# Performance work log

Hardware: AMD Instinct MI355X
Metric: run time of the kernel (lower is better)

Reference implementation:

```python
import jax, jax.numpy as jnp
import numpy as np


def setup_inputs() -> dict:
    key = jax.random.key(0)
    k1, k2, k3, k4 = jax.random.split(key, 4)
    T, H, E, I = 4096, 1024, 8, 3584
    return {
        "hidden_states": jax.random.normal(k1, (T, H), dtype=jnp.float32),
        "gate_w": jax.random.normal(k2, (H, E), dtype=jnp.float32) * 0.02,
        "w1": jax.random.normal(k3, (E, H, I), dtype=jnp.float32) * 0.02,
        "w2": jax.random.normal(k4, (E, I, H), dtype=jnp.float32) * 0.02,
        "top_k": 2,
    }


def reference(hidden_states, gate_w, w1, w2, top_k):
    # Router: logits -> softmax -> top-k -> renormalize (Mixtral / vLLM fused_moe)
    router_logits = hidden_states @ gate_w                    # [T, E]
    probs = jax.nn.softmax(router_logits, axis=-1)
    top_vals, top_idx = jax.lax.top_k(probs, top_k)           # [T, K]
    top_vals = top_vals / jnp.sum(top_vals, axis=-1, keepdims=True)
    E = gate_w.shape[1]
    # Dense per-(token, expert) combine weights, zero for non-selected experts
    dense_w = jnp.sum(jax.nn.one_hot(top_idx, E, dtype=hidden_states.dtype)
                      * top_vals[..., None], axis=1)          # [T, E]
    # Expert MLP: silu(x @ w1[e]) @ w2[e], weighted by routing probs
    act = jax.nn.silu(jnp.einsum('th,ehi->tei', hidden_states, w1))  # [T, E, I]
    act = act * dense_w[:, :, None]
    out = jnp.einsum('tei,eih->th', act, w2)                  # [T, H]
    return out
```

## Files before the change

kernel.cpp:

```cpp
#include <hip/hip_runtime.h>
#include <hip/hip_bf16.h>

#define T_TOK 4096
#define H_DIM 1024
#define E_NUM 8
#define I_DIM 3584
#define NPAIR (T_TOK * 2)
#define MAX_RT 72

#define BM 128
#define BN 128
#define BK 64

typedef __attribute__((ext_vector_type(8))) short bf16x8;
typedef __attribute__((ext_vector_type(4))) float f32x4;
typedef __attribute__((ext_vector_type(8))) unsigned short ushort8_t;
typedef __attribute__((ext_vector_type(4))) unsigned short ushort4_t;

__device__ __forceinline__ unsigned short f2bf(float x) {
  unsigned int u = __float_as_uint(x);
  unsigned int r = (u + 0x7FFFu + ((u >> 16) & 1u)) >> 16;
  return (unsigned short)r;
}

__device__ __forceinline__ void gload16(const void* g, unsigned short* l) {
  __builtin_amdgcn_global_load_lds(
      (const __attribute__((address_space(1))) void*)g,
      (__attribute__((address_space(3))) void*)l, 16, 0, 0);
}

__device__ __forceinline__ void transpose_body2(const float* __restrict__ src,
                                                unsigned short* __restrict__ dst,
                                                int R, int C, int e, int c0, int r0,
                                                char* smem) {
  float (*tile)[65] = reinterpret_cast<float (*)[65]>(smem);
  const float* s = src + (size_t)e * R * C;
  unsigned short* d = dst + (size_t)e * R * C;
  const int th = threadIdx.x;
  const int tr = th >> 4;
  const int tc4 = (th & 15) * 4;
  const int wc = th >> 3;
  const int wr = (th & 7) * 8;
  ushort8_t oA[2];
#pragma unroll
  for (int it = 0; it < 4; ++it) {
    const int r = it * 16 + tr;
    float4 v = *reinterpret_cast<const float4*>(s + (size_t)(r0 + r) * C + c0 + tc4);
    tile[r][tc4] = v.x; tile[r][tc4 + 1] = v.y; tile[r][tc4 + 2] = v.z; tile[r][tc4 + 3] = v.w;
  }
  __syncthreads();
#pragma unroll
  for (int it = 0; it < 2; ++it) {
    const int c = it * 32 + wc;
#pragma unroll
    for (int j = 0; j < 8; ++j) oA[it][j] = f2bf(tile[wr + j][c]);
  }
  __syncthreads();
#pragma unroll
  for (int it = 0; it < 4; ++it) {
    const int r = it * 16 + tr;
    float4 v = *reinterpret_cast<const float4*>(s + (size_t)(r0 + 64 + r) * C + c0 + tc4);
    tile[r][tc4] = v.x; tile[r][tc4 + 1] = v.y; tile[r][tc4 + 2] = v.z; tile[r][tc4 + 3] = v.w;
  }
  __syncthreads();
#pragma unroll
  for (int it = 0; it < 2; ++it) {
    const int c = it * 32 + wc;
    ushort8_t oB;
#pragma unroll
    for (int j = 0; j < 8; ++j) oB[j] = f2bf(tile[wr + j][c]);
    *reinterpret_cast<ushort8_t*>(d + (size_t)(c0 + c) * R + r0 + wr) = oA[it];
    *reinterpret_cast<ushort8_t*>(d + (size_t)(c0 + c) * R + r0 + 64 + wr) = oB;
  }
}

__device__ __forceinline__ void router_body(const float* __restrict__ hs,
                                            const float* __restrict__ gw,
                                            unsigned short* __restrict__ hsb,
                                            int* __restrict__ eid, float* __restrict__ wgt,
                                            int* __restrict__ counts, int rbid, char* smem) {
  float* s_gw = reinterpret_cast<float*>(smem);
  int* s_cnt = reinterpret_cast<int*>(smem + 32768);
  const int th = threadIdx.x;
  for (int u = th; u < 2048; u += 256) {
    const f32x4 v = *reinterpret_cast<const f32x4*>(gw + u * 4);
    *reinterpret_cast<f32x4*>(&s_gw[(u ^ ((u >> 3) & 7)) * 4]) = v;
  }
  if (th < E_NUM) s_cnt[th] = 0;
  __syncthreads();

  const int l = th & 63, w = th >> 6;
#pragma unroll 1
  for (int tt = 0; tt < 4; ++tt) {
    const int t = rbid * 16 + w * 4 + tt;
    const float* hrow = hs + (size_t)t * H_DIM;
    unsigned short* brow = hsb + (size_t)t * H_DIM;
    float acc[E_NUM];
#pragma unroll
    for (int e = 0; e < E_NUM; ++e) acc[e] = 0.f;
#pragma unroll
    for (int i = 0; i < 4; ++i) {
      const int h0 = i * 256 + l * 4;
      const f32x4 x = *reinterpret_cast<const f32x4*>(hrow + h0);
      ushort4_t o = { f2bf(x[0]), f2bf(x[1]), f2bf(x[2]), f2bf(x[3]) };
      *reinterpret_cast<ushort4_t*>(brow + h0) = o;
#pragma unroll
      for (int j = 0; j < 4; ++j) {
        const int h = h0 + j;
        const int p0 = (h * 2) ^ ((h >> 2) & 7);
        const f32x4 g0 = *reinterpret_cast<const f32x4*>(&s_gw[p0 * 4]);
        const f32x4 g1 = *reinterpret_cast<const f32x4*>(&s_gw[(p0 ^ 1) * 4]);
        acc[0] += x[j] * g0[0]; acc[1] += x[j] * g0[1];
        acc[2] += x[j] * g0[2]; acc[3] += x[j] * g0[3];
        acc[4] += x[j] * g1[0]; acc[5] += x[j] * g1[1];
        acc[6] += x[j] * g1[2]; acc[7] += x[j] * g1[3];
      }
    }
#pragma unroll
    for (int e = 0; e < E_NUM; ++e) {
#pragma unroll
      for (int off = 1; off < 64; off <<= 1) acc[e] += __shfl_xor(acc[e], off);
    }
    if (l == 0) {
      int i1 = 0;
#pragma unroll
      for (int e = 1; e < E_NUM; ++e) if (acc[e] > acc[i1]) i1 = e;
      int i2 = (i1 == 0) ? 1 : 0;
#pragma unroll
      for (int e = 0; e < E_NUM; ++e) if (e != i1 && acc[e] > acc[i2]) i2 = e;
      const float e2 = __expf(acc[i2] - acc[i1]);
      const float inv = 1.f / (1.f + e2);
      eid[t * 2] = i1;     wgt[t * 2] = inv;
      eid[t * 2 + 1] = i2; wgt[t * 2 + 1] = e2 * inv;
      atomicAdd(&s_cnt[i1], 1);
      atomicAdd(&s_cnt[i2], 1);
    }
  }
  __syncthreads();
  if (th < E_NUM && s_cnt[th] > 0) atomicAdd(&counts[th], s_cnt[th]);
}

__global__ __launch_bounds__(256) void prep_kernel(
    const float* __restrict__ w1, const float* __restrict__ w2,
    const float* __restrict__ hs, const float* __restrict__ gw,
    unsigned short* __restrict__ w1t, unsigned short* __restrict__ w2t,
    unsigned short* __restrict__ hsb,
    int* __restrict__ eid, float* __restrict__ wgt, int* __restrict__ counts) {
  __shared__ char smem[33024];
  const int bid = blockIdx.x;
  if (bid < 256) {
    router_body(hs, gw, hsb, eid, wgt, counts, bid, smem);
    return;
  }
  const int idx = bid - 256;
  const float* src;
  unsigned short* dst;
  int R, C, e, c0, r0;
  if (idx < 3584) {
    e = idx / 448; const int rem = idx % 448;
    R = H_DIM; C = I_DIM; c0 = (rem % 56) * 64; r0 = (rem / 56) * 128;
    src = w1; dst = w1t;
  } else {
    const int i2 = idx - 3584;
    e = i2 / 448; const int rem = i2 % 448;
    R = I_DIM; C = H_DIM; c0 = (rem % 16) * 64; r0 = (rem / 16) * 128;
    src = w2; dst = w2t;
  }
  transpose_body2(src, dst, R, C, e, c0, r0, smem);
}

__global__ void scatter_kernel(const int* __restrict__ eid, const int* __restrict__ counts,
                               int* __restrict__ fill, int* __restrict__ rowmap,
                               int* __restrict__ posmap) {
  __shared__ int hist[E_NUM], base[E_NUM];
  const int th = threadIdx.x;
  const int p = blockIdx.x * 256 + th;
  if (th < E_NUM) hist[th] = 0;
  __syncthreads();
  const int e = eid[p];
  const int rloc = atomicAdd(&hist[e], 1);
  __syncthreads();
  if (th < E_NUM) base[th] = (hist[th] > 0) ? atomicAdd(&fill[th], hist[th]) : 0;
  __syncthreads();
  int off = 0;
#pragma unroll
  for (int i = 0; i < E_NUM; ++i) off += (i < e) ? counts[i] : 0;
  const int pos = off + base[e] + rloc;
  rowmap[pos] = p;
  posmap[p] = pos;
}

__global__ void combine_kernel(const float* __restrict__ res, const int* __restrict__ posmap,
                               float* __restrict__ out) {
  const int t = blockIdx.x;
  const int th = threadIdx.x;
  const int a = posmap[t * 2];
  const int b = posmap[t * 2 + 1];
  const float4 va = *reinterpret_cast<const float4*>(res + (size_t)a * H_DIM + th * 4);
  const float4 vb = *reinterpret_cast<const float4*>(res + (size_t)b * H_DIM + th * 4);
  float4 o = { va.x + vb.x, va.y + vb.y, va.z + vb.z, va.w + vb.w };
  *reinterpret_cast<float4*>(out + (size_t)t * H_DIM + th * 4) = o;
}

template <int MODE, int NCT>
__launch_bounds__(256, 4)
__global__ void moe_gemm(const unsigned short* __restrict__ hsb,
                         const unsigned short* __restrict__ wt,
                         const unsigned short* __restrict__ act_in,
                         unsigned short* __restrict__ act_out,
                         float* __restrict__ res,
                         const int* __restrict__ counts,
                         const int* __restrict__ rowmap,
                         const float* __restrict__ wgt) {
  constexpr int KD = (MODE == 0) ? H_DIM : I_DIM;
  constexpr int NWG = MAX_RT * NCT;
  constexpr int CHUNK = NWG / 8;

  __shared__ unsigned short As[BM * BK];
  __shared__ unsigned short Bs[BN * BK];
  __shared__ float s_w[BM];

  const int bid = blockIdx.x;
  const int wgid = (bid & 7) * CHUNK + (bid >> 3);
  int rt, ct;
  if (MODE == 0) {
    const int l = wgid % CHUNK;
    const int sg = l / 36;
    const int q = l % 36;
    rt = (wgid / CHUNK) * 9 + q % 9;
    ct = sg * 4 + q / 9;
  } else {
    const int c9 = (wgid / CHUNK) * 9;
    const int l = wgid % CHUNK;
    if (l < 64) {
      const int band = l >> 4, inner = l & 15;
      rt = c9 + band * 2 + (inner & 1);
      ct = inner >> 1;
    } else {
      rt = c9 + 8;
      ct = l - 64;
    }
  }

  int e = -1, loc_rt = 0, off_e = 0, cnt = 0;
  {
    int acc_t = 0, off = 0;
#pragma unroll
    for (int ee = 0; ee < E_NUM; ++ee) {
      const int c = counts[ee];
      const int nt = (c + BM - 1) >> 7;
      if (e < 0 && rt < acc_t + nt) { e = ee; loc_rt = rt - acc_t; off_e = off; cnt = c; }
      acc_t += nt; off += c;
    }
  }
  if (e < 0) return;

  const int cnt_local = min(BM, cnt - loc_rt * BM);
  const int r_base = off_e + loc_rt * BM;
  const int th = threadIdx.x;
  const int lane = th & 63, wid = th >> 6;

  if (MODE == 1 && th < BM) {
    int r = loc_rt * BM + th;
    if (r >= cnt) r = cnt - 1;
    s_w[th] = wgt[rowmap[off_e + r]];
  }

  const int n0 = ct * BN;
  const unsigned short* wbase = wt + (size_t)e * ((size_t)I_DIM * H_DIM) + (size_t)n0 * KD;

  const int srow = lane >> 3;
  const int cg = (lane & 7) ^ srow;
  const char* aptr[4];
  const char* bptr[4];
#pragma unroll
  for (int i = 0; i < 4; ++i) {
    const int r = i * 32 + wid * 8 + srow;
    const int rr = (r < cnt_local) ? r : (cnt_local - 1);
    if (MODE == 0) {
      const int tok = rowmap[off_e + loc_rt * BM + rr] >> 1;
      aptr[i] = (const char*)(hsb + (size_t)tok * H_DIM) + cg * 16;
    } else {
      aptr[i] = (const char*)(act_in + (size_t)(r_base + rr) * I_DIM) + cg * 16;
    }
    bptr[i] = (const char*)(wbase + (size_t)r * KD) + cg * 16;
  }
  unsigned short* dstA[4];
  unsigned short* dstB[4];
#pragma unroll
  for (int i = 0; i < 4; ++i) {
    dstA[i] = &As[(i * 32 + wid * 8) * BK];
    dstB[i] = &Bs[(i * 32 + wid * 8) * BK];
  }

  f32x4 acc[4][4];
#pragma unroll
  for (int m = 0; m < 4; ++m)
#pragma unroll
    for (int n = 0; n < 4; ++n) acc[m][n] = (f32x4){0.f, 0.f, 0.f, 0.f};

  const int wm = (wid >> 1) * 64;
  const int wn = (wid & 1) * 64;
  const int fr = lane & 15;
  const int fq = lane >> 4;
  const int sxor = fr & 7;

  for (int k0 = 0; k0 < KD; k0 += BK) {
    const int kb = k0 * 2;
#pragma unroll
    for (int i = 0; i < 4; ++i) gload16(aptr[i] + kb, dstA[i]);
#pragma unroll
    for (int i = 0; i < 4; ++i) gload16(bptr[i] + kb, dstB[i]);
    __syncthreads();

#pragma unroll
    for (int kk = 0; kk < 2; ++kk) {
      bf16x8 af[4], bf[4];
#pragma unroll
      for (int m = 0; m < 4; ++m)
        af[m] = *reinterpret_cast<const bf16x8*>(
            &As[(wm + m * 16 + fr) * BK + ((kk * 4 + fq) ^ sxor) * 8]);
#pragma unroll
      for (int n = 0; n < 4; ++n)
        bf[n] = *reinterpret_cast<const bf16x8*>(
            &Bs[(wn + n * 16 + fr) * BK + ((kk * 4 + fq) ^ sxor) * 8]);
#pragma unroll
      for (int m = 0; m < 4; ++m)
#pragma unroll
        for (int n = 0; n < 4; ++n)
          acc[m][n] = __builtin_amdgcn_mfma_f32_16x16x32_bf16(af[m], bf[n], acc[m][n], 0, 0, 0);
    }
    __syncthreads();
  }

#pragma unroll
  for (int m = 0; m < 4; ++m) {
    const int row = wm + m * 16 + fq * 4;
#pragma unroll
    for (int n = 0; n < 4; ++n) {
      const int col = wn + n * 16 + fr;
#pragma unroll
      for (int r = 0; r < 4; ++r) {
        const int rw = row + r;
        if (rw < cnt_local) {
          const float x = acc[m][n][r];
          if (MODE == 0) {
            const float s = x / (1.f + __expf(-x));
            act_out[(size_t)(r_base + rw) * I_DIM + n0 + col] = f2bf(s);
          } else {
            res[(size_t)(r_base + rw) * H_DIM + n0 + col] = x * s_w[rw];
          }
        }
      }
    }
  }
}

extern "C" void kernel_launch(void* const* d_in, const int* in_sizes, int n_in,
                              void* d_out, int out_size, void* d_ws, size_t ws_size,
                              hipStream_t stream) {
  const float* hs = (const float*)d_in[0];
  const float* gw = (const float*)d_in[1];
  const float* w1 = (const float*)d_in[2];
  const float* w2 = (const float*)d_in[3];
  float* out = (float*)d_out;

  char* ws = (char*)d_ws;
  const size_t WMAT = (size_t)E_NUM * I_DIM * H_DIM * 2;
  unsigned short* w1t = (unsigned short*)ws;
  unsigned short* w2t = (unsigned short*)(ws + WMAT);
  unsigned short* act = (unsigned short*)(ws + 2 * WMAT);
  unsigned short* hsb = (unsigned short*)(ws + 3 * WMAT);
  float* res = (float*)w1t;
  char* small = ws + 3 * WMAT + (size_t)T_TOK * H_DIM * 2;
  int* eid = (int*)small;
  float* wgt = (float*)(small + NPAIR * 4);
  int* rowmap = (int*)(small + 2 * NPAIR * 4);
  int* posmap = (int*)(small + 3 * NPAIR * 4);
  int* counts = (int*)(small + 4 * NPAIR * 4);
  int* fill = counts + 8;

  hipMemsetAsync(counts, 0, 16 * sizeof(int), stream);

  prep_kernel<<<7424, 256, 0, stream>>>(w1, w2, hs, gw, w1t, w2t, hsb, eid, wgt, counts);
  scatter_kernel<<<NPAIR / 256, 256, 0, stream>>>(eid, counts, fill, rowmap, posmap);

  moe_gemm<0, I_DIM / BN><<<MAX_RT * (I_DIM / BN), 256, 0, stream>>>(
      hsb, w1t, nullptr, act, nullptr, counts, rowmap, wgt);
  moe_gemm<1, H_DIM / BN><<<MAX_RT * (H_DIM / BN), 256, 0, stream>>>(
      hsb, w2t, act, nullptr, res, counts, rowmap, wgt);

  combine_kernel<<<T_TOK, 256, 0, stream>>>(res, posmap, out);
}
```

Measured before the change: 251.3 us.

## Overlap w2 transpose/convert with first expert GEMM in one launch

Moves the w2 fp32-to-bf16 transpose out of the prep kernel and appends its blocks to the first grouped GEMM launch, so the memory-bound conversion runs alongside the compute-bound GEMM0 tiles. The prep kernel now handles only the router and the w1 transpose, which shortens the critical path before GEMM0. The risk is that transpose blocks compete with GEMM tiles for bandwidth and CUs. The shared-memory layout is also reshaped so both roles fit in one kernel, which could change occupancy.

Measured after the change: 244.6 us, median of 2. -2.6%, faster.

```diff
diff --git a/kernel.cpp b/kernel.cpp
--- a/kernel.cpp
+++ b/kernel.cpp
@@ -11,6 +11,8 @@
 #define BM 128
 #define BN 128
 #define BK 64
+#define G0_NWG (MAX_RT * (I_DIM / BN))
+#define WT_NB 3584
 
 typedef __attribute__((ext_vector_type(8))) short bf16x8;
 typedef __attribute__((ext_vector_type(4))) float f32x4;
@@ -140,11 +142,10 @@
   if (th < E_NUM && s_cnt[th] > 0) atomicAdd(&counts[th], s_cnt[th]);
 }
 
-__global__ __launch_bounds__(256) void prep_kernel(
-    const float* __restrict__ w1, const float* __restrict__ w2,
-    const float* __restrict__ hs, const float* __restrict__ gw,
-    unsigned short* __restrict__ w1t, unsigned short* __restrict__ w2t,
-    unsigned short* __restrict__ hsb,
+__global__ __launch_bounds__(256) void prep1_kernel(
+    const float* __restrict__ w1, const float* __restrict__ hs,
+    const float* __restrict__ gw,
+    unsigned short* __restrict__ w1t, unsigned short* __restrict__ hsb,
     int* __restrict__ eid, float* __restrict__ wgt, int* __restrict__ counts) {
   __shared__ char smem[33024];
   const int bid = blockIdx.x;
@@ -153,20 +154,8 @@
     return;
   }
   const int idx = bid - 256;
-  const float* src;
-  unsigned short* dst;
-  int R, C, e, c0, r0;
-  if (idx < 3584) {
-    e = idx / 448; const int rem = idx % 448;
-    R = H_DIM; C = I_DIM; c0 = (rem % 56) * 64; r0 = (rem / 56) * 128;
-    src = w1; dst = w1t;
-  } else {
-    const int i2 = idx - 3584;
-    e = i2 / 448; const int rem = i2 % 448;
-    R = I_DIM; C = H_DIM; c0 = (rem % 16) * 64; r0 = (rem / 16) * 128;
-    src = w2; dst = w2t;
-  }
-  transpose_body2(src, dst, R, C, e, c0, r0, smem);
+  const int e = idx / 448, rem = idx % 448;
+  transpose_body2(w1, w1t, H_DIM, I_DIM, e, (rem % 56) * 64, (rem / 56) * 128, smem);
 }
 
 __global__ void scatter_kernel(const int* __restrict__ eid, const int* __restrict__ counts,
@@ -202,17 +191,138 @@
   *reinterpret_cast<float4*>(out + (size_t)t * H_DIM + th * 4) = o;
 }
 
-template <int MODE, int NCT>
+__global__ __launch_bounds__(256, 4) void gemm0_w2t_kernel(
+    const unsigned short* __restrict__ hsb, const unsigned short* __restrict__ w1t,
+    unsigned short* __restrict__ act,
+    const float* __restrict__ w2, unsigned short* __restrict__ w2t,
+    const int* __restrict__ counts, const int* __restrict__ rowmap) {
+  __shared__ char smem[(BM * BK + BN * BK) * 2];
+  const int bid = blockIdx.x;
+  if (bid >= G0_NWG) {
+    const int idx = bid - G0_NWG;
+    const int e = idx / 448, rem = idx % 448;
+    transpose_body2(w2, w2t, I_DIM, H_DIM, e, (rem % 16) * 64, (rem / 16) * 128, smem);
+    return;
+  }
+  unsigned short* As = reinterpret_cast<unsigned short*>(smem);
+  unsigned short* Bs = As + BM * BK;
+
+  constexpr int CHUNK = G0_NWG / 8;
+  const int wgid = (bid & 7) * CHUNK + (bid >> 3);
+  const int l = wgid % CHUNK;
+  const int sg = l / 36;
+  const int q = l % 36;
+  const int rt = (wgid / CHUNK) * 9 + q % 9;
+  const int ct = sg * 4 + q / 9;
+
+  int e = -1, loc_rt = 0, off_e = 0, cnt = 0;
+  {
+    int acc_t = 0, off = 0;
+#pragma unroll
+    for (int ee = 0; ee < E_NUM; ++ee) {
+      const int c = counts[ee];
+      const int nt = (c + BM - 1) >> 7;
+      if (e < 0 && rt < acc_t + nt) { e = ee; loc_rt = rt - acc_t; off_e = off; cnt = c; }
+      acc_t += nt; off += c;
+    }
+  }
+  if (e < 0) return;
+
+  const int cnt_local = min(BM, cnt - loc_rt * BM);
+  const int r_base = off_e + loc_rt * BM;
+  const int th = threadIdx.x;
+  const int lane = th & 63, wid = th >> 6;
+
+  const int n0 = ct * BN;
+  const unsigned short* wbase = w1t + (size_t)e * ((size_t)I_DIM * H_DIM) + (size_t)n0 * H_DIM;
+
+  const int srow = lane >> 3;
+  const int cg = (lane & 7) ^ srow;
+  const char* aptr[4];
+  const char* bptr[4];
+#pragma unroll
+  for (int i = 0; i < 4; ++i) {
+    const int r = i * 32 + wid * 8 + srow;
+    const int rr = (r < cnt_local) ? r : (cnt_local - 1);
+    const int tok = rowmap[off_e + loc_rt * BM + rr] >> 1;
+    aptr[i] = (const char*)(hsb + (size_t)tok * H_DIM) + cg * 16;
+    bptr[i] = (const char*)(wbase + (size_t)r * H_DIM) + cg * 16;
+  }
+  unsigned short* dstA[4];
+  unsigned short* dstB[4];
+#pragma unroll
+  for (int i = 0; i < 4; ++i) {
+    dstA[i] = &As[(i * 32 + wid * 8) * BK];
+    dstB[i] = &Bs[(i * 32 + wid * 8) * BK];
+  }
+
+  f32x4 acc[4][4];
+#pragma unroll
+  for (int m = 0; m < 4; ++m)
+#pragma unroll
+    for (int n = 0; n < 4; ++n) acc[m][n] = (f32x4){0.f, 0.f, 0.f, 0.f};
+
+  const int wm = (wid >> 1) * 64;
+  const int wn = (wid & 1) * 64;
+  const int fr = lane & 15;
+  const int fq = lane >> 4;
+  const int sxor = fr & 7;
+
+  for (int k0 = 0; k0 < H_DIM; k0 += BK) {
+    const int kb = k0 * 2;
+#pragma unroll
+    for (int i = 0; i < 4; ++i) gload16(aptr[i] + kb, dstA[i]);
+#pragma unroll
+    for (int i = 0; i < 4; ++i) gload16(bptr[i] + kb, dstB[i]);
+    __syncthreads();
+
+#pragma unroll
+    for (int kk = 0; kk < 2; ++kk) {
+      bf16x8 af[4], bf[4];
+#pragma unroll
+      for (int m = 0; m < 4; ++m)
+        af[m] = *reinterpret_cast<const bf16x8*>(
+            &As[(wm + m * 16 + fr) * BK + ((kk * 4 + fq) ^ sxor) * 8]);
+#pragma unroll
+      for (int n = 0; n < 4; ++n)
+        bf[n] = *reinterpret_cast<const bf16x8*>(
+            &Bs[(wn + n * 16 + fr) * BK + ((kk * 4 + fq) ^ sxor) * 8]);
+#pragma unroll
+      for (int m = 0; m < 4; ++m)
+#pragma unroll
+        for (int n = 0; n < 4; ++n)
+          acc[m][n] = __builtin_amdgcn_mfma_f32_16x16x32_bf16(af[m], bf[n], acc[m][n], 0, 0, 0);
+    }
+    __syncthreads();
+  }
+
+#pragma unroll
+  for (int m = 0; m < 4; ++m) {
+    const int row = wm + m * 16 + fq * 4;
+#pragma unroll
+    for (int n = 0; n < 4; ++n) {
+      const int col = wn + n * 16 + fr;
+#pragma unroll
+      for (int r = 0; r < 4; ++r) {
+        const int rw = row + r;
+        if (rw < cnt_local) {
+          const float x = acc[m][n][r];
+          const float s = x / (1.f + __expf(-x));
+          act[(size_t)(r_base + rw) * I_DIM + n0 + col] = f2bf(s);
+        }
+      }
+    }
+  }
+}
+
 __launch_bounds__(256, 4)
-__global__ void moe_gemm(const unsigned short* __restrict__ hsb,
-                         const unsigned short* __restrict__ wt,
-                         const unsigned short* __restrict__ act_in,
-                         unsigned short* __restrict__ act_out,
-                         float* __restrict__ res,
-                         const int* __restrict__ counts,
-                         const int* __restrict__ rowmap,
-                         const float* __restrict__ wgt) {
-  constexpr int KD = (MODE == 0) ? H_DIM : I_DIM;
+__global__ void moe_gemm1(const unsigned short* __restrict__ w2t,
+                          const unsigned short* __restrict__ act_in,
+                          float* __restrict__ res,
+                          const int* __restrict__ counts,
+                          const int* __restrict__ rowmap,
+                          const float* __restrict__ wgt) {
+  constexpr int NCT = H_DIM / BN;
   constexpr int NWG = MAX_RT * NCT;
   constexpr int CHUNK = NWG / 8;
 
@@ -223,13 +333,7 @@
   const int bid = blockIdx.x;
   const int wgid = (bid & 7) * CHUNK + (bid >> 3);
   int rt, ct;
-  if (MODE == 0) {
-    const int l = wgid % CHUNK;
-    const int sg = l / 36;
-    const int q = l % 36;
-    rt = (wgid / CHUNK) * 9 + q % 9;
-    ct = sg * 4 + q / 9;
-  } else {
+  {
     const int c9 = (wgid / CHUNK) * 9;
     const int l = wgid % CHUNK;
     if (l < 64) {
@@ -260,14 +364,14 @@
   const int th = threadIdx.x;
   const int lane = th & 63, wid = th >> 6;
 
-  if (MODE == 1 && th < BM) {
+  if (th < BM) {
     int r = loc_rt * BM + th;
     if (r >= cnt) r = cnt - 1;
     s_w[th] = wgt[rowmap[off_e + r]];
   }
 
   const int n0 = ct * BN;
-  const unsigned short* wbase = wt + (size_t)e * ((size_t)I_DIM * H_DIM) + (size_t)n0 * KD;
+  const unsigned short* wbase = w2t + (size_t)e * ((size_t)I_DIM * H_DIM) + (size_t)n0 * I_DIM;
 
   const int srow = lane >> 3;
   const int cg = (lane & 7) ^ srow;
@@ -277,13 +381,8 @@
   for (int i = 0; i < 4; ++i) {
     const int r = i * 32 + wid * 8 + srow;
     const int rr = (r < cnt_local) ? r : (cnt_local - 1);
-    if (MODE == 0) {
-      const int tok = rowmap[off_e + loc_rt * BM + rr] >> 1;
-      aptr[i] = (const char*)(hsb + (size_t)tok * H_DIM) + cg * 16;
-    } else {
-      aptr[i] = (const char*)(act_in + (size_t)(r_base + rr) * I_DIM) + cg * 16;
-    }
-    bptr[i] = (const char*)(wbase + (size_t)r * KD) + cg * 16;
+    aptr[i] = (const char*)(act_in + (size_t)(r_base + rr) * I_DIM) + cg * 16;
+    bptr[i] = (const char*)(wbase + (size_t)r * I_DIM) + cg * 16;
   }
   unsigned short* dstA[4];
   unsigned short* dstB[4];
@@ -305,7 +404,7 @@
   const int fq = lane >> 4;
   const int sxor = fr & 7;
 
-  for (int k0 = 0; k0 < KD; k0 += BK) {
+  for (int k0 = 0; k0 < I_DIM; k0 += BK) {
     const int kb = k0 * 2;
 #pragma unroll
     for (int i = 0; i < 4; ++i) gload16(aptr[i] + kb, dstA[i]);
@@ -342,15 +441,8 @@
 #pragma unroll
       for (int r = 0; r < 4; ++r) {
         const int rw = row + r;
-        if (rw < cnt_local) {
-          const float x = acc[m][n][r];
-          if (MODE == 0) {
-            const float s = x / (1.f + __expf(-x));
-            act_out[(size_t)(r_base + rw) * I_DIM + n0 + col] = f2bf(s);
-          } else {
-            res[(size_t)(r_base + rw) * H_DIM + n0 + col] = x * s_w[rw];
-          }
-        }
+        if (rw < cnt_local)
+          res[(size_t)(r_base + rw) * H_DIM + n0 + col] = acc[m][n][r] * s_w[rw];
       }
     }
   }
@@ -382,13 +474,13 @@
 
   hipMemsetAsync(counts, 0, 16 * sizeof(int), stream);
 
-  prep_kernel<<<7424, 256, 0, stream>>>(w1, w2, hs, gw, w1t, w2t, hsb, eid, wgt, counts);
+  prep1_kernel<<<256 + WT_NB, 256, 0, stream>>>(w1, hs, gw, w1t, hsb, eid, wgt, counts);
   scatter_kernel<<<NPAIR / 256, 256, 0, stream>>>(eid, counts, fill, rowmap, posmap);
 
-  moe_gemm<0, I_DIM / BN><<<MAX_RT * (I_DIM / BN), 256, 0, stream>>>(
-      hsb, w1t, nullptr, act, nullptr, counts, rowmap, wgt);
-  moe_gemm<1, H_DIM / BN><<<MAX_RT * (H_DIM / BN), 256, 0, stream>>>(
-      hsb, w2t, act, nullptr, res, counts, rowmap, wgt);
+  gemm0_w2t_kernel<<<G0_NWG + WT_NB, 256, 0, stream>>>(
+      hsb, w1t, act, w2, w2t, counts, rowmap);
+  moe_gemm1<<<MAX_RT * (H_DIM / BN), 256, 0, stream>>>(
+      w2t, act, res, counts, rowmap, wgt);
 
   combine_kernel<<<T_TOK, 256, 0, stream>>>(res, posmap, out);
 }
```
